# Kernel optimization log

Hardware: AMD Instinct MI355X
Metric: run time of the kernel (lower is better)

Reference implementation:

```python
import jax, jax.numpy as jnp
import numpy as np

IN_F, OUT_F, N_CH, N_TILES, PTS = 256, 256, 1024, 1024, 256
OMEGA = 30.0


def setup_inputs() -> dict:
    key = jax.random.key(0)
    kx, kw, kb, ki = jax.random.split(key, 4)
    bound = float(np.sqrt(6.0 / IN_F) / OMEGA)  # SIREN-style init (is_first=False)
    x = jax.random.normal(kx, (N_TILES, PTS, IN_F), dtype=jnp.float32)
    weight = jax.random.uniform(kw, (N_CH, IN_F, OUT_F), dtype=jnp.float32,
                                minval=-bound, maxval=bound)
    bias = jax.random.uniform(kb, (1, 1, OUT_F), dtype=jnp.float32,
                              minval=-bound, maxval=bound)
    indices = jax.random.randint(ki, (N_TILES,), 0, N_CH, dtype=jnp.int64)
    return {"x": x, "weight": weight, "bias": bias, "indices": indices}


def reference(x, weight, bias, indices):
    # gather per-tile weight slice then batched matmul: [T,P,I] @ [T,I,O] -> [T,P,O]
    w = weight[indices]                      # [T, I, O]
    out = jnp.einsum('tpi,tio->tpo', x, w) + bias[0]
    return jnp.sin(OMEGA * out)
```

## Files before the change

kernel.cpp:

```cpp
#include <hip/hip_runtime.h>

typedef _Float16 half8_t __attribute__((ext_vector_type(8)));
typedef _Float16 half4_t __attribute__((ext_vector_type(4)));
typedef float    float4_t __attribute__((ext_vector_type(4)));

#define N_TILES 1024
#define PTS     256
#define IN_F    256
#define OUT_F   256
#define BM      64
#define BK      32
#define LDK     40
#define NSTEP   (IN_F / BK)
#define OMEGA_C 30.0f

#define BARRIER() do {                                        \
    asm volatile("s_waitcnt lgkmcnt(0)" ::: "memory");        \
    __builtin_amdgcn_s_barrier();                             \
    asm volatile("" ::: "memory");                            \
  } while (0)

#define BSWZ(g, n) (((g) ^ (((n) >> 3) & 3)))

__global__ __launch_bounds__(512, 4)
void siren_tile_gemm(const float* __restrict__ x,
                     const float* __restrict__ w,
                     const float* __restrict__ bias,
                     const void* __restrict__ idx_raw,
                     float* __restrict__ out) {
  __shared__ __align__(16) _Float16 Al[2][BM][LDK];
  __shared__ __align__(16) _Float16 Bl[2][OUT_F][LDK];

  const int tid = threadIdx.x;

  const int b    = blockIdx.x;
  const int xcd  = b & 7;
  const int rest = b >> 3;
  const int tile = xcd + 8 * (rest >> 2);
  const int mq   = rest & 3;

  const int hiw  = ((const int*)idx_raw)[2 * (tid & 63) + 1];
  const bool is32 = __any(hiw != 0);
  const int ch = is32 ? ((const int*)idx_raw)[tile]
                      : (int)(((const long long*)idx_raw)[tile]);

  const float* __restrict__ Xg = x + (size_t)tile * (PTS * IN_F) + (size_t)mq * BM * IN_F;
  const float* __restrict__ Wg = w + (size_t)ch * (IN_F * OUT_F);
  float*       __restrict__ Og = out + (size_t)tile * (PTS * OUT_F) + (size_t)mq * BM * OUT_F;

  const int a_row = tid >> 3;
  const int a_col = (tid & 7) * 4;
  const int b_kb  = tid >> 6;
  const int b_nb  = tid & 63;

  float4_t acc[2][4];
#pragma unroll
  for (int m = 0; m < 2; ++m)
#pragma unroll
    for (int n = 0; n < 4; ++n)
      acc[m][n] = (float4_t){0.f, 0.f, 0.f, 0.f};

  float4_t aS[2];
  float4_t bS[2][4];

#define ISSUE(slot, s)                                                          \
  do {                                                                          \
    const int k0_ = (s) * BK;                                                   \
    aS[slot] = *(const float4_t*)(Xg + (size_t)a_row * IN_F + k0_ + a_col);     \
    _Pragma("unroll")                                                           \
    for (int j = 0; j < 4; ++j)                                                 \
      bS[slot][j] = *(const float4_t*)(Wg + (size_t)(k0_ + b_kb * 4 + j) * OUT_F + b_nb * 4); \
  } while (0)

#define STORE_LDS(slot, buf)                                                    \
  do {                                                                          \
    half4_t ha_ = {(_Float16)aS[slot].x, (_Float16)aS[slot].y,                  \
                   (_Float16)aS[slot].z, (_Float16)aS[slot].w};                 \
    *(half4_t*)&Al[buf][a_row][a_col] = ha_;                                    \
    _Pragma("unroll")                                                           \
    for (int i = 0; i < 4; ++i) {                                               \
      const int n_ = b_nb * 4 + i;                                              \
      half4_t hb_ = {(_Float16)bS[slot][0][i], (_Float16)bS[slot][1][i],        \
                     (_Float16)bS[slot][2][i], (_Float16)bS[slot][3][i]};       \
      *(half4_t*)&Bl[buf][n_][BSWZ(b_kb >> 1, n_) * 8 + (b_kb & 1) * 4] = hb_;  \
    }                                                                           \
  } while (0)

  ISSUE(0, 0);
  ISSUE(1, 1);
  STORE_LDS(0, 0);
  BARRIER();

  const int lane = tid & 63;
  const int wid  = tid >> 6;
  const int wm   = (wid >> 2) * 32;
  const int wn   = (wid & 3) * 64;
  const int fr   = lane & 15;
  const int kg   = lane >> 4;

#pragma unroll
  for (int s = 0; s < NSTEP; ++s) {
    const int cur = s & 1;

    half8_t af[2], bf[4];
#pragma unroll
    for (int m = 0; m < 2; ++m)
      af[m] = *(const half8_t*)&Al[cur][wm + m * 16 + fr][kg * 8];
#pragma unroll
    for (int n = 0; n < 4; ++n) {
      const int r = wn + n * 16 + fr;
      bf[n] = *(const half8_t*)&Bl[cur][r][BSWZ(kg, r) * 8];
    }

#pragma unroll
    for (int m = 0; m < 2; ++m)
#pragma unroll
      for (int n = 0; n < 4; ++n)
        acc[m][n] = __builtin_amdgcn_mfma_f32_16x16x32_f16(af[m], bf[n], acc[m][n], 0, 0, 0);

    if (s + 2 < NSTEP) ISSUE(cur, s + 2);
    if (s + 1 < NSTEP) {
      STORE_LDS(cur ^ 1, cur ^ 1);
      BARRIER();
    }
  }

  float bv[4];
#pragma unroll
  for (int n = 0; n < 4; ++n) bv[n] = OMEGA_C * bias[wn + n * 16 + fr];

#pragma unroll
  for (int m = 0; m < 2; ++m) {
#pragma unroll
    for (int n = 0; n < 4; ++n) {
#pragma unroll
      for (int j = 0; j < 4; ++j) {
        const int row = wm + m * 16 + kg * 4 + j;
        const int col = wn + n * 16 + fr;
        Og[(size_t)row * OUT_F + col] = __sinf(fmaf(OMEGA_C, acc[m][n][j], bv[n]));
      }
    }
  }
}

extern "C" void kernel_launch(void* const* d_in, const int* in_sizes, int n_in,
                              void* d_out, int out_size, void* d_ws, size_t ws_size,
                              hipStream_t stream) {
  const float* x    = (const float*)d_in[0];
  const float* w    = (const float*)d_in[1];
  const float* bias = (const float*)d_in[2];
  const void*  idx  = d_in[3];
  float*       out  = (float*)d_out;

  siren_tile_gemm<<<N_TILES * 4, 512, 0, stream>>>(x, w, bias, idx, out);
}
```

Measured before the change: 166.2 us.

## Retile per-tile GEMM into 128x64 blocks with 256 threads and XCD remap

Changes each block from a 64-row by full-256-column output tile (512 threads) to a 128-row by 64-column tile (256 threads), launching 8192 blocks. The block-to-tile mapping is reworked so that the eight sub-blocks of one tile stay on the same XCD, which should improve L2 reuse of x and the weight slice. Prefetch depth drops to one stage issued at the top of each step. B loads become scalar coalesced reads, and the B swizzle is replaced by padding, with each B fragment read as two half4 loads. In exchange, x rows are now read by four blocks instead of one, and scalar weight loads cost more instructions per element.

```diff
diff --git a/kernel.cpp b/kernel.cpp
--- a/kernel.cpp
+++ b/kernel.cpp
@@ -4,15 +4,9 @@
 typedef _Float16 half4_t __attribute__((ext_vector_type(4)));
 typedef float    float4_t __attribute__((ext_vector_type(4)));
 
-#define N_TILES 1024
-#define PTS     256
-#define IN_F    256
-#define OUT_F   256
-#define BM      64
-#define BK      32
-#define LDK     40
-#define NSTEP   (IN_F / BK)
 #define OMEGA_C 30.0f
+#define LDKA 40
+#define LDKB 36
 
 #define BARRIER() do {                                        \
     asm volatile("s_waitcnt lgkmcnt(0)" ::: "memory");        \
@@ -20,124 +14,135 @@
     asm volatile("" ::: "memory");                            \
   } while (0)
 
-#define BSWZ(g, n) (((g) ^ (((n) >> 3) & 3)))
-
-__global__ __launch_bounds__(512, 4)
+__global__ __launch_bounds__(256, 4)
 void siren_tile_gemm(const float* __restrict__ x,
                      const float* __restrict__ w,
                      const float* __restrict__ bias,
                      const void* __restrict__ idx_raw,
                      float* __restrict__ out) {
-  __shared__ __align__(16) _Float16 Al[2][BM][LDK];
-  __shared__ __align__(16) _Float16 Bl[2][OUT_F][LDK];
+  __shared__ __align__(16) _Float16 Al[2][128][LDKA];
+  __shared__ __align__(16) _Float16 Bl[2][64][LDKB];
 
   const int tid = threadIdx.x;
 
-  const int b    = blockIdx.x;
-  const int xcd  = b & 7;
-  const int rest = b >> 3;
-  const int tile = xcd + 8 * (rest >> 2);
-  const int mq   = rest & 3;
+  const int b  = blockIdx.x;
+  const int u  = (b & 7) * 1024 + (b >> 3);
+  const int tile = u >> 3;
+  const int mh   = (u >> 2) & 1;
+  const int nq   = u & 3;
 
-  const int hiw  = ((const int*)idx_raw)[2 * (tid & 63) + 1];
+  const int hiw   = ((const int*)idx_raw)[2 * (tid & 63) + 1];
   const bool is32 = __any(hiw != 0);
   const int ch = is32 ? ((const int*)idx_raw)[tile]
                       : (int)(((const long long*)idx_raw)[tile]);
 
-  const float* __restrict__ Xg = x + (size_t)tile * (PTS * IN_F) + (size_t)mq * BM * IN_F;
-  const float* __restrict__ Wg = w + (size_t)ch * (IN_F * OUT_F);
-  float*       __restrict__ Og = out + (size_t)tile * (PTS * OUT_F) + (size_t)mq * BM * OUT_F;
+  const float* __restrict__ Xg = x + (size_t)tile * 65536 + (size_t)mh * 128 * 256;
+  const float* __restrict__ Wg = w + (size_t)ch * 65536 + nq * 64;
+  float*       __restrict__ Og = out + (size_t)tile * 65536 + (size_t)mh * 128 * 256 + nq * 64;
 
   const int a_row = tid >> 3;
   const int a_col = (tid & 7) * 4;
-  const int b_kb  = tid >> 6;
-  const int b_nb  = tid & 63;
+  const int b_kq = tid >> 6;
+  const int b_n  = tid & 63;
 
-  float4_t acc[2][4];
+  float4_t acc[4][2];
 #pragma unroll
-  for (int m = 0; m < 2; ++m)
+  for (int m = 0; m < 4; ++m)
 #pragma unroll
-    for (int n = 0; n < 4; ++n)
+    for (int n = 0; n < 2; ++n)
       acc[m][n] = (float4_t){0.f, 0.f, 0.f, 0.f};
 
-  float4_t aS[2];
-  float4_t bS[2][4];
+  float4_t xr[4];
+  float    wb[8];
 
-#define ISSUE(slot, s)                                                          \
+#define ISSUE_A(s)                                                              \
   do {                                                                          \
-    const int k0_ = (s) * BK;                                                   \
-    aS[slot] = *(const float4_t*)(Xg + (size_t)a_row * IN_F + k0_ + a_col);     \
+    const int k0_ = (s) * 32;                                                   \
     _Pragma("unroll")                                                           \
-    for (int j = 0; j < 4; ++j)                                                 \
-      bS[slot][j] = *(const float4_t*)(Wg + (size_t)(k0_ + b_kb * 4 + j) * OUT_F + b_nb * 4); \
+    for (int p_ = 0; p_ < 4; ++p_)                                              \
+      xr[p_] = *(const float4_t*)(Xg + (size_t)(a_row + 32 * p_) * 256 + k0_ + a_col); \
   } while (0)
 
-#define STORE_LDS(slot, buf)                                                    \
+#define ISSUE_B(s)                                                              \
   do {                                                                          \
-    half4_t ha_ = {(_Float16)aS[slot].x, (_Float16)aS[slot].y,                  \
-                   (_Float16)aS[slot].z, (_Float16)aS[slot].w};                 \
-    *(half4_t*)&Al[buf][a_row][a_col] = ha_;                                    \
+    const int k0_ = (s) * 32;                                                   \
     _Pragma("unroll")                                                           \
-    for (int i = 0; i < 4; ++i) {                                               \
-      const int n_ = b_nb * 4 + i;                                              \
-      half4_t hb_ = {(_Float16)bS[slot][0][i], (_Float16)bS[slot][1][i],        \
-                     (_Float16)bS[slot][2][i], (_Float16)bS[slot][3][i]};       \
-      *(half4_t*)&Bl[buf][n_][BSWZ(b_kb >> 1, n_) * 8 + (b_kb & 1) * 4] = hb_;  \
+    for (int j_ = 0; j_ < 4; ++j_) {                                            \
+      wb[j_]     = Wg[(size_t)(k0_ + b_kq * 4 + j_) * 256 + b_n];               \
+      wb[j_ + 4] = Wg[(size_t)(k0_ + 16 + b_kq * 4 + j_) * 256 + b_n];          \
     }                                                                           \
   } while (0)
 
-  ISSUE(0, 0);
-  ISSUE(1, 1);
-  STORE_LDS(0, 0);
+#define STORE_AB(buf)                                                           \
+  do {                                                                          \
+    _Pragma("unroll")                                                           \
+    for (int p_ = 0; p_ < 4; ++p_) {                                            \
+      half4_t h_ = {(_Float16)xr[p_].x, (_Float16)xr[p_].y,                     \
+                    (_Float16)xr[p_].z, (_Float16)xr[p_].w};                    \
+      *(half4_t*)&Al[buf][a_row + 32 * p_][a_col] = h_;                         \
+    }                                                                           \
+    half4_t hb0_ = {(_Float16)wb[0], (_Float16)wb[1],                           \
+                    (_Float16)wb[2], (_Float16)wb[3]};                          \
+    half4_t hb1_ = {(_Float16)wb[4], (_Float16)wb[5],                           \
+                    (_Float16)wb[6], (_Float16)wb[7]};                          \
+    *(half4_t*)&Bl[buf][b_n][b_kq * 4]      = hb0_;                             \
+    *(half4_t*)&Bl[buf][b_n][16 + b_kq * 4] = hb1_;                             \
+  } while (0)
+
+  ISSUE_A(0);
+  ISSUE_B(0);
+  STORE_AB(0);
   BARRIER();
 
   const int lane = tid & 63;
   const int wid  = tid >> 6;
-  const int wm   = (wid >> 2) * 32;
-  const int wn   = (wid & 3) * 64;
+  const int wm   = (wid >> 1) * 64;
+  const int wn   = (wid & 1) * 32;
   const int fr   = lane & 15;
   const int kg   = lane >> 4;
 
+#pragma unroll 2
+  for (int s = 0; s < 8; ++s) {
+    const int cur = s & 1;
+    if (s + 1 < 8) { ISSUE_A(s + 1); ISSUE_B(s + 1); }
+
+    half8_t af[4], bf[2];
 #pragma unroll
-  for (int s = 0; s < NSTEP; ++s) {
-    const int cur = s & 1;
-
-    half8_t af[2], bf[4];
-#pragma unroll
-    for (int m = 0; m < 2; ++m)
+    for (int m = 0; m < 4; ++m)
       af[m] = *(const half8_t*)&Al[cur][wm + m * 16 + fr][kg * 8];
 #pragma unroll
-    for (int n = 0; n < 4; ++n) {
+    for (int n = 0; n < 2; ++n) {
       const int r = wn + n * 16 + fr;
-      bf[n] = *(const half8_t*)&Bl[cur][r][BSWZ(kg, r) * 8];
+      half4_t lo = *(const half4_t*)&Bl[cur][r][kg * 8];
+      half4_t hi = *(const half4_t*)&Bl[cur][r][kg * 8 + 4];
+      bf[n] = (half8_t){lo.x, lo.y, lo.z, lo.w, hi.x, hi.y, hi.z, hi.w};
     }
 
 #pragma unroll
-    for (int m = 0; m < 2; ++m)
+    for (int m = 0; m < 4; ++m)
 #pragma unroll
-      for (int n = 0; n < 4; ++n)
+      for (int n = 0; n < 2; ++n)
         acc[m][n] = __builtin_amdgcn_mfma_f32_16x16x32_f16(af[m], bf[n], acc[m][n], 0, 0, 0);
 
-    if (s + 2 < NSTEP) ISSUE(cur, s + 2);
-    if (s + 1 < NSTEP) {
-      STORE_LDS(cur ^ 1, cur ^ 1);
+    if (s + 1 < 8) {
+      STORE_AB(cur ^ 1);
       BARRIER();
     }
   }
 
-  float bv[4];
+  float bv[2];
 #pragma unroll
-  for (int n = 0; n < 4; ++n) bv[n] = OMEGA_C * bias[wn + n * 16 + fr];
+  for (int n = 0; n < 2; ++n) bv[n] = OMEGA_C * bias[nq * 64 + wn + n * 16 + fr];
 
 #pragma unroll
-  for (int m = 0; m < 2; ++m) {
+  for (int m = 0; m < 4; ++m) {
 #pragma unroll
-    for (int n = 0; n < 4; ++n) {
+    for (int n = 0; n < 2; ++n) {
 #pragma unroll
       for (int j = 0; j < 4; ++j) {
         const int row = wm + m * 16 + kg * 4 + j;
         const int col = wn + n * 16 + fr;
-        Og[(size_t)row * OUT_F + col] = __sinf(fmaf(OMEGA_C, acc[m][n][j], bv[n]));
+        Og[(size_t)row * 256 + col] = __sinf(fmaf(OMEGA_C, acc[m][n][j], bv[n]));
       }
     }
   }
@@ -152,5 +157,5 @@
   const void*  idx  = d_in[3];
   float*       out  = (float*)d_out;
 
-  siren_tile_gemm<<<N_TILES * 4, 512, 0, stream>>>(x, w, bias, idx, out);
+  siren_tile_gemm<<<8192, 256, 0, stream>>>(x, w, bias, idx, out);
 }
```

New measurement: 171.3 us. 3.1% more time.
